# Kernel optimization log

Measured on AMD Instinct MI355X. Metric: run time of the kernel, lower is better.

Reference implementation:

```python
import jax, jax.numpy as jnp
import numpy as np

N_HEAD = 16

def setup_inputs() -> dict:
    key = jax.random.key(0)
    k1, k2, k3 = jax.random.split(key, 3)
    B, T, C = 4, 2048, 1024
    x = jax.random.normal(k1, (B, T, C), dtype=jnp.float32)
    W_attn = jax.random.normal(k2, (C, 3 * C), dtype=jnp.float32) * (1.0 / np.sqrt(C))
    W_proj = jax.random.normal(k3, (C, C), dtype=jnp.float32) * (1.0 / np.sqrt(C))
    return {"x": x, "W_attn": W_attn, "W_proj": W_proj}

def reference(x, W_attn, W_proj):
    B, T, C = x.shape
    H = N_HEAD
    D = C // H  # head_dim
    qkv = x @ W_attn                      # (B, T, 3C)
    q, k, v = jnp.split(qkv, 3, axis=-1)
    # (B, T, C) -> (B, H, T, D)
    q = q.reshape(B, T, H, D).transpose(0, 2, 1, 3)
    k = k.reshape(B, T, H, D).transpose(0, 2, 1, 3)
    v = v.reshape(B, T, H, D).transpose(0, 2, 1, 3)
    scale = 1.0 / np.sqrt(D)
    att = jnp.einsum('bhqd,bhkd->bhqk', q, k) * scale  # (B, H, T, T)
    causal = jnp.tril(jnp.ones((T, T), dtype=bool))
    att = jnp.where(causal[None, None, :, :], att, -jnp.inf)
    att = jax.nn.softmax(att, axis=-1)
    y = jnp.einsum('bhqk,bhkd->bhqd', att, v)          # (B, H, T, D)
    y = y.transpose(0, 2, 1, 3).reshape(B, T, C)
    y = y @ W_proj
    return y
```

## Files before the change

kernel.cpp:

```cpp
#include <hip/hip_runtime.h>
#include <hip/hip_bf16.h>
#include <stdint.h>

typedef __attribute__((ext_vector_type(8))) __bf16 bf16x8;
typedef __attribute__((ext_vector_type(4))) __bf16 bf16x4;
typedef __attribute__((ext_vector_type(4))) float f32x4;

static __device__ __forceinline__ ushort f2bf(float f) {
  union { float f; uint32_t u; } v; v.f = f;
  uint32_t u = v.u;
  u += 0x7fffu + ((u >> 16) & 1u);
  return (ushort)(u >> 16);
}

static __device__ __forceinline__ void gl_lds16(const ushort* g, ushort* l) {
  __builtin_amdgcn_global_load_lds(
      (__attribute__((address_space(1))) unsigned int*)(g),
      (__attribute__((address_space(3))) unsigned int*)(l), 16, 0, 0);
}

__global__ __launch_bounds__(256) void cast_f32_bf16(
    const float* __restrict__ in, ushort* __restrict__ out, int n) {
  int i = (blockIdx.x * 256 + threadIdx.x) * 4;
  if (i >= n) return;
  float4 v = *(const float4*)&in[i];
  ushort4 o;
  o.x = f2bf(v.x); o.y = f2bf(v.y); o.z = f2bf(v.z); o.w = f2bf(v.w);
  *(ushort4*)&out[i] = o;
}

__global__ __launch_bounds__(256) void transpose_cast(
    const float* __restrict__ W, ushort* __restrict__ Wt, int K, int N) {
  __shared__ ushort tile[32][33];
  int n0 = blockIdx.x * 32, k0 = blockIdx.y * 32;
  int tx = threadIdx.x, ty = threadIdx.y;
  #pragma unroll
  for (int r = ty; r < 32; r += 8)
    tile[r][tx] = f2bf(W[(size_t)(k0 + r) * N + n0 + tx]);
  __syncthreads();
  #pragma unroll
  for (int r = ty; r < 32; r += 8)
    Wt[(size_t)(n0 + r) * K + k0 + tx] = tile[tx][r];
}

template <int MODE>
__global__ __launch_bounds__(512, 2) void gemm_bt(
    const ushort* __restrict__ A, const ushort* __restrict__ Bt,
    float* __restrict__ Cf, int M, int N, int K,
    ushort* __restrict__ Qo, ushort* __restrict__ Ko, ushort* __restrict__ Vo) {
  __shared__ ushort smem[49152];
  const int tid = threadIdx.x;
  const int lane = tid & 63;
  const int w = tid >> 6;
  const int wm = (w >> 2) * 128;
  const int wn = (w & 3) * 32;
  const int lr = lane & 15, kg = lane >> 4;
  const int fid = blockIdx.x;
  const int m0 = (((fid & 7) << 2) + ((fid >> 3) & 3)) << 8;
  const int n0 = (fid >> 5) << 7;

  auto stageA = [&](int buf, int tile, int q) {
    const int k0 = tile << 6;
    const int rowb = q * 32 + (w >> 2) * 128 + (w & 3) * 8;
    gl_lds16(&A[(size_t)(m0 + rowb + (lane >> 3)) * K + k0 +
                (((lane & 7) ^ (lane >> 3)) << 3)],
             &smem[buf * 16384 + rowb * 64]);
  };
  auto stageB = [&](int buf, int tile, int h) {
    const int k0 = tile << 6;
    const int rowb = h * 64 + w * 8;
    gl_lds16(&Bt[(size_t)(n0 + rowb + (lane >> 3)) * K + k0 +
                 (((lane & 7) ^ (lane >> 3)) << 3)],
             &smem[32768 + buf * 8192 + rowb * 64]);
  };

  f32x4 zero = {0.f, 0.f, 0.f, 0.f};
  f32x4 acc[8][2];
  #pragma unroll
  for (int i = 0; i < 8; i++)
    #pragma unroll
    for (int j = 0; j < 2; j++) acc[i][j] = zero;

  const int cs0 = ((kg ^ (lr & 7)) << 3);
  const int cs1 = (((4 + kg) ^ (lr & 7)) << 3);

  const int nt = K >> 6;
  stageA(0, 0, 0); stageA(0, 0, 1); stageA(0, 0, 2); stageA(0, 0, 3);
  stageB(0, 0, 0); stageB(0, 0, 1);
  stageA(1, 1, 0); stageA(1, 1, 1); stageA(1, 1, 2);
  stageB(1, 1, 0); stageB(1, 1, 1);

  for (int t = 0; t < nt; ++t) {
    const int cur = t & 1, nxt = cur ^ 1;
    const int ab = cur * 16384, bb = 32768 + cur * 8192;
    if (t + 1 < nt)
      asm volatile("s_waitcnt vmcnt(5)" ::: "memory");
    else
      asm volatile("s_waitcnt vmcnt(0)" ::: "memory");
    __builtin_amdgcn_s_barrier();
    asm volatile("" ::: "memory");
    if (t + 1 < nt) stageA(nxt, t + 1, 3);
    bf16x8 bfr[2][2], af[2][2];
    #pragma unroll
    for (int j = 0; j < 2; ++j) {
      const int R = wn + j * 16 + lr;
      bfr[j][0] = *(const bf16x8*)&smem[bb + R * 64 + cs0];
      bfr[j][1] = *(const bf16x8*)&smem[bb + R * 64 + cs1];
    }
    #pragma unroll
    for (int il = 0; il < 2; ++il) {
      const int R = wm + il * 16 + lr;
      af[il][0] = *(const bf16x8*)&smem[ab + R * 64 + cs0];
      af[il][1] = *(const bf16x8*)&smem[ab + R * 64 + cs1];
    }
    asm volatile("s_waitcnt lgkmcnt(0)" ::: "memory");
    __builtin_amdgcn_sched_barrier(0);
    __builtin_amdgcn_s_setprio(1);
    #pragma unroll
    for (int il = 0; il < 2; ++il)
      #pragma unroll
      for (int j = 0; j < 2; ++j) {
        acc[il][j] = __builtin_amdgcn_mfma_f32_16x16x32_bf16(
            af[il][0], bfr[j][0], acc[il][j], 0, 0, 0);
        acc[il][j] = __builtin_amdgcn_mfma_f32_16x16x32_bf16(
            af[il][1], bfr[j][1], acc[il][j], 0, 0, 0);
      }
    __builtin_amdgcn_s_setprio(0);
    __builtin_amdgcn_s_barrier();
    asm volatile("" ::: "memory");
    #pragma unroll
    for (int p = 1; p < 4; ++p) {
      if (t + 2 < nt) {
        stageA(cur, t + 2, p - 1);
        if (p < 3) stageB(cur, t + 2, p - 1);
      }
      bf16x8 a2[2][2];
      #pragma unroll
      for (int il = 0; il < 2; ++il) {
        const int R = wm + (2 * p + il) * 16 + lr;
        a2[il][0] = *(const bf16x8*)&smem[ab + R * 64 + cs0];
        a2[il][1] = *(const bf16x8*)&smem[ab + R * 64 + cs1];
      }
      asm volatile("s_waitcnt lgkmcnt(0)" ::: "memory");
      __builtin_amdgcn_sched_barrier(0);
      __builtin_amdgcn_s_setprio(1);
      #pragma unroll
      for (int il = 0; il < 2; ++il)
        #pragma unroll
        for (int j = 0; j < 2; ++j) {
          acc[2 * p + il][j] = __builtin_amdgcn_mfma_f32_16x16x32_bf16(
              a2[il][0], bfr[j][0], acc[2 * p + il][j], 0, 0, 0);
          acc[2 * p + il][j] = __builtin_amdgcn_mfma_f32_16x16x32_bf16(
              a2[il][1], bfr[j][1], acc[2 * p + il][j], 0, 0, 0);
        }
      __builtin_amdgcn_s_setprio(0);
      __builtin_amdgcn_s_barrier();
      asm volatile("" ::: "memory");
    }
  }

  if (MODE == 2) {
    #pragma unroll
    for (int i = 0; i < 8; i++)
      #pragma unroll
      for (int j = 0; j < 2; j++)
        #pragma unroll
        for (int r = 0; r < 4; r++) {
          int mrow = m0 + wm + i * 16 + kg * 4 + r;
          int ncol = n0 + wn + j * 16 + lr;
          Cf[(size_t)mrow * N + ncol] = acc[i][j][r];
        }
  } else {
    __syncthreads();
    ushort* Ls = smem + w * 5120;
    const int nb = n0 + wn;
    const int which = nb >> 10;
    const int bb2 = (m0 + wm) >> 11;
    const int hh = (nb & 1023) >> 6;
    const int d0 = nb & 63;
    const size_t bh = (size_t)(bb2 * 16 + hh);
    const int t0 = (m0 + wm) & 2047;
    if (which == 2) {
      #pragma unroll
      for (int i = 0; i < 8; i++)
        #pragma unroll
        for (int j = 0; j < 2; j++)
          #pragma unroll
          for (int r = 0; r < 4; r++)
            Ls[(j * 16 + lr) * 136 + (i * 16 + kg * 4 + r)] =
                f2bf(acc[i][j][r]);
      #pragma unroll
      for (int it = 0; it < 8; it++) {
        const int cid = it * 64 + lane;
        const int d = cid >> 4, chk = cid & 15;
        bf16x8 v = *(const bf16x8*)&Ls[d * 136 + chk * 8];
        *(bf16x8*)&Vo[(bh * 64 + d0 + d) * 2048 + t0 + chk * 8] = v;
      }
    } else {
      const float sc = (which == 0) ? 0.18033688011112042f : 1.0f;
      #pragma unroll
      for (int i = 0; i < 8; i++)
        #pragma unroll
        for (int j = 0; j < 2; j++)
          #pragma unroll
          for (int r = 0; r < 4; r++)
            Ls[(i * 16 + kg * 4 + r) * 40 + (j * 16 + lr)] =
                f2bf(acc[i][j][r] * sc);
      ushort* dst = (which == 0) ? Qo : Ko;
      #pragma unroll
      for (int it = 0; it < 8; it++) {
        const int cid = it * 64 + lane;
        const int row = cid >> 2, chk = cid & 3;
        bf16x8 v = *(const bf16x8*)&Ls[row * 40 + chk * 8];
        *(bf16x8*)&dst[(bh * 2048 + t0 + row) * 64 + d0 + chk * 8] = v;
      }
    }
  }
}

__global__ __launch_bounds__(256, 4) void attn_fwd(
    const ushort* __restrict__ Q, const ushort* __restrict__ Kc,
    const ushort* __restrict__ Vt, ushort* __restrict__ Y) {
  __shared__ ushort Ks[2][64][64];
  __shared__ ushort Vs[2][64][64];
  __shared__ ushort Ps[4][16][64];
  const int tid = threadIdx.x;
  const int lane = tid & 63, w = tid >> 6;
  const int lr = lane & 15, kg = lane >> 4;
  int blk = blockIdx.x;
  blk = (blk & 7) * 128 + (blk >> 3);
  const int pair = blk & 15;
  const int bh = blk >> 4;
  const ushort* Qp = Q + (size_t)bh * 2048 * 64;
  const ushort* Kp = Kc + (size_t)bh * 2048 * 64;
  const ushort* Vp = Vt + (size_t)bh * 64 * 2048;
  const int b = bh >> 4, h = bh & 15;
  const int swz = (lr & 14) << 3;
  char* PsB = (char*)&Ps[w][0][0];
  const int srow = lane >> 3, schunk = lane & 7;
  const int cs0 = (kg ^ (lr & 7)) << 3;
  const int cs1 = ((kg ^ 4) ^ (lr & 7)) << 3;
  f32x4 zero = {0.f, 0.f, 0.f, 0.f};

  auto stageKV = [&](int buf, int k0) {
    #pragma unroll
    for (int c = 0; c < 2; c++) {
      const int rbase = w * 16 + c * 8;
      const int r = rbase + srow;
      gl_lds16(&Kp[(size_t)(k0 + r) * 64 + ((schunk ^ (r & 7)) << 3)],
               &Ks[buf][rbase][0]);
      gl_lds16(&Vp[(size_t)r * 2048 + k0 + ((schunk ^ (r & 7)) << 3)],
               &Vs[buf][rbase][0]);
    }
  };

  for (int half = 0; half < 2; half++) {
    const int j = half ? (31 - pair) : pair;
    const int q0b = j << 6;
    const int qw0 = q0b + w * 16;
    bf16x8 qf0 = *(const bf16x8*)&Qp[(size_t)(qw0 + lr) * 64 + kg * 8];
    bf16x8 qf1 = *(const bf16x8*)&Qp[(size_t)(qw0 + lr) * 64 + 32 + kg * 8];
    f32x4 o[4];
    #pragma unroll
    for (int dt = 0; dt < 4; dt++) o[dt] = zero;
    float lsum = 0.f;

    stageKV(0, 0);
    __syncthreads();
    for (int k0 = 0; k0 <= q0b; k0 += 64) {
      const int cur = (k0 >> 6) & 1;
      if (k0 < q0b) stageKV(cur ^ 1, k0 + 64);

      f32x4 s[4];
      #pragma unroll
      for (int ct = 0; ct < 4; ct++) {
        bf16x8 kf0 = *(const bf16x8*)&Ks[cur][ct * 16 + lr][cs0];
        bf16x8 kf1 = *(const bf16x8*)&Ks[cur][ct * 16 + lr][cs1];
        f32x4 z = zero;
        z = __builtin_amdgcn_mfma_f32_16x16x32_bf16(kf0, qf0, z, 0, 0, 0);
        z = __builtin_amdgcn_mfma_f32_16x16x32_bf16(kf1, qf1, z, 0, 0, 0);
        s[ct] = z;
      }
      if (k0 == q0b) {
        const int qrow = qw0 + lr;
        #pragma unroll
        for (int ct = 0; ct < 4; ct++)
          #pragma unroll
          for (int r = 0; r < 4; r++) {
            int kj = k0 + ct * 16 + kg * 4 + r;
            s[ct][r] = (kj > qrow) ? -1e30f : s[ct][r];
          }
      }
      #pragma unroll
      for (int ct = 0; ct < 4; ct++) {
        float p0 = exp2f(s[ct][0]);
        float p1 = exp2f(s[ct][1]);
        float p2 = exp2f(s[ct][2]);
        float p3 = exp2f(s[ct][3]);
        lsum += (p0 + p1) + (p2 + p3);
        bf16x4 pk = {(__bf16)p0, (__bf16)p1, (__bf16)p2, (__bf16)p3};
        *(bf16x4*)(PsB + lr * 128 + ((ct * 32 + kg * 8) ^ swz)) = pk;
      }
      bf16x8 pa0 = *(const bf16x8*)(PsB + lr * 128 + ((kg * 16) ^ swz));
      bf16x8 pa1 = *(const bf16x8*)(PsB + lr * 128 + ((64 + kg * 16) ^ swz));
      #pragma unroll
      for (int dt = 0; dt < 4; dt++) {
        bf16x8 vf0 = *(const bf16x8*)&Vs[cur][dt * 16 + lr][cs0];
        bf16x8 vf1 = *(const bf16x8*)&Vs[cur][dt * 16 + lr][cs1];
        f32x4 t = o[dt];
        t = __builtin_amdgcn_mfma_f32_16x16x32_bf16(pa0, vf0, t, 0, 0, 0);
        t = __builtin_amdgcn_mfma_f32_16x16x32_bf16(pa1, vf1, t, 0, 0, 0);
        o[dt] = t;
      }
      __syncthreads();
    }

    lsum += __shfl_xor(lsum, 16);
    lsum += __shfl_xor(lsum, 32);
    float inv = 1.f / lsum;
    f32x4 ib;
    #pragma unroll
    for (int r = 0; r < 4; r++) ib[r] = __shfl(inv, kg * 4 + r);
    #pragma unroll
    for (int dt = 0; dt < 4; dt++) {
      #pragma unroll
      for (int r = 0; r < 4; r++) {
        size_t t = (size_t)qw0 + kg * 4 + r;
        Y[((size_t)b * 2048 + t) * 1024 + h * 64 + dt * 16 + lr] =
            f2bf(o[dt][r] * ib[r]);
      }
    }
  }
}

extern "C" void kernel_launch(void* const* d_in, const int* in_sizes, int n_in,
                              void* d_out, int out_size, void* d_ws,
                              size_t ws_size, hipStream_t stream) {
  const float* x = (const float*)d_in[0];
  const float* Wa = (const float*)d_in[1];
  const float* Wp = (const float*)d_in[2];
  float* out = (float*)d_out;

  char* ws = (char*)d_ws;
  size_t off = 0;
  auto carve = [&](size_t bytes) {
    void* p = ws + off;
    off += (bytes + 255) & ~(size_t)255;
    return p;
  };
  ushort* Xb = (ushort*)carve(8192ull * 1024 * 2);
  ushort* Wat = (ushort*)carve(3072ull * 1024 * 2);
  ushort* Wpt = (ushort*)carve(1024ull * 1024 * 2);
  ushort* Qh = (ushort*)carve(64ull * 2048 * 64 * 2);
  ushort* Kh = (ushort*)carve(64ull * 2048 * 64 * 2);
  ushort* Vt = (ushort*)carve(64ull * 64 * 2048 * 2);
  ushort* Yb = (ushort*)carve(8192ull * 1024 * 2);

  cast_f32_bf16<<<8192, 256, 0, stream>>>(x, Xb, 8192 * 1024);
  transpose_cast<<<dim3(96, 32), dim3(32, 8), 0, stream>>>(Wa, Wat, 1024, 3072);
  transpose_cast<<<dim3(32, 32), dim3(32, 8), 0, stream>>>(Wp, Wpt, 1024, 1024);
  gemm_bt<1><<<768, 512, 0, stream>>>(Xb, Wat, nullptr, 8192, 3072, 1024, Qh,
                                      Kh, Vt);
  attn_fwd<<<1024, 256, 0, stream>>>(Qh, Kh, Vt, Yb);
  gemm_bt<2><<<256, 512, 0, stream>>>(Yb, Wpt, out, 8192, 1024, 1024, nullptr,
                                      nullptr, nullptr);
}
```

Before: 177.0 us.

## Shrink GEMM tiles to 128x128 with 4 waves and restructure pipeline

Changes the GEMM from 256x128 tiles with 8 waves to 128x128 tiles with 4 waves, each wave computing a 64x64 sub-tile. The grid doubles, and the software pipeline is reorganised into two half-phases that alternate loading A and B. The epilogue now writes full 64-wide head chunks to Q/K/V. The goal is more blocks for better CU load balance and a larger per-wave tile for register reuse, at the cost of lower arithmetic intensity per block and more global traffic.

```diff
diff --git a/kernel.cpp b/kernel.cpp
--- a/kernel.cpp
+++ b/kernel.cpp
@@ -44,68 +44,69 @@
 }
 
 template <int MODE>
-__global__ __launch_bounds__(512, 2) void gemm_bt(
+__global__ __launch_bounds__(256, 2) void gemm_bt(
     const ushort* __restrict__ A, const ushort* __restrict__ Bt,
     float* __restrict__ Cf, int M, int N, int K,
     ushort* __restrict__ Qo, ushort* __restrict__ Ko, ushort* __restrict__ Vo) {
-  __shared__ ushort smem[49152];
+  __shared__ ushort smem[32768];
   const int tid = threadIdx.x;
   const int lane = tid & 63;
   const int w = tid >> 6;
-  const int wm = (w >> 2) * 128;
-  const int wn = (w & 3) * 32;
+  const int wm = (w >> 1) * 64, wn = (w & 1) * 64;
   const int lr = lane & 15, kg = lane >> 4;
   const int fid = blockIdx.x;
-  const int m0 = (((fid & 7) << 2) + ((fid >> 3) & 3)) << 8;
-  const int n0 = (fid >> 5) << 7;
+  const int m0 = (((fid & 7) << 3) + ((fid >> 3) & 7)) << 7;
+  const int n0 = (fid >> 6) << 7;
 
   auto stageA = [&](int buf, int tile, int q) {
     const int k0 = tile << 6;
-    const int rowb = q * 32 + (w >> 2) * 128 + (w & 3) * 8;
+    const int rowb = q * 32 + w * 8;
     gl_lds16(&A[(size_t)(m0 + rowb + (lane >> 3)) * K + k0 +
                 (((lane & 7) ^ (lane >> 3)) << 3)],
-             &smem[buf * 16384 + rowb * 64]);
+             &smem[buf * 8192 + rowb * 64]);
   };
-  auto stageB = [&](int buf, int tile, int h) {
+  auto stageB = [&](int buf, int tile, int q) {
     const int k0 = tile << 6;
-    const int rowb = h * 64 + w * 8;
+    const int rowb = q * 32 + w * 8;
     gl_lds16(&Bt[(size_t)(n0 + rowb + (lane >> 3)) * K + k0 +
                  (((lane & 7) ^ (lane >> 3)) << 3)],
-             &smem[32768 + buf * 8192 + rowb * 64]);
+             &smem[16384 + buf * 8192 + rowb * 64]);
   };
 
   f32x4 zero = {0.f, 0.f, 0.f, 0.f};
-  f32x4 acc[8][2];
+  f32x4 acc[4][4];
   #pragma unroll
-  for (int i = 0; i < 8; i++)
-    #pragma unroll
-    for (int j = 0; j < 2; j++) acc[i][j] = zero;
+  for (int i = 0; i < 4; i++)
+    #pragma unroll
+    for (int j = 0; j < 4; j++) acc[i][j] = zero;
 
   const int cs0 = ((kg ^ (lr & 7)) << 3);
   const int cs1 = (((4 + kg) ^ (lr & 7)) << 3);
 
   const int nt = K >> 6;
+  stageB(0, 0, 0); stageB(0, 0, 1); stageB(0, 0, 2); stageB(0, 0, 3);
   stageA(0, 0, 0); stageA(0, 0, 1); stageA(0, 0, 2); stageA(0, 0, 3);
-  stageB(0, 0, 0); stageB(0, 0, 1);
-  stageA(1, 1, 0); stageA(1, 1, 1); stageA(1, 1, 2);
-  stageB(1, 1, 0); stageB(1, 1, 1);
+  stageB(1, 1, 0); stageB(1, 1, 1); stageB(1, 1, 2); stageB(1, 1, 3);
 
   for (int t = 0; t < nt; ++t) {
     const int cur = t & 1, nxt = cur ^ 1;
-    const int ab = cur * 16384, bb = 32768 + cur * 8192;
+    const int ab = cur * 8192, bbo = 16384 + cur * 8192;
     if (t + 1 < nt)
-      asm volatile("s_waitcnt vmcnt(5)" ::: "memory");
+      asm volatile("s_waitcnt vmcnt(4)" ::: "memory");
     else
       asm volatile("s_waitcnt vmcnt(0)" ::: "memory");
     __builtin_amdgcn_s_barrier();
     asm volatile("" ::: "memory");
-    if (t + 1 < nt) stageA(nxt, t + 1, 3);
-    bf16x8 bfr[2][2], af[2][2];
-    #pragma unroll
-    for (int j = 0; j < 2; ++j) {
+    if (t + 1 < nt) {
+      stageA(nxt, t + 1, 0); stageA(nxt, t + 1, 1);
+      stageA(nxt, t + 1, 2); stageA(nxt, t + 1, 3);
+    }
+    bf16x8 bfr[4][2], af[2][2];
+    #pragma unroll
+    for (int j = 0; j < 4; ++j) {
       const int R = wn + j * 16 + lr;
-      bfr[j][0] = *(const bf16x8*)&smem[bb + R * 64 + cs0];
-      bfr[j][1] = *(const bf16x8*)&smem[bb + R * 64 + cs1];
+      bfr[j][0] = *(const bf16x8*)&smem[bbo + R * 64 + cs0];
+      bfr[j][1] = *(const bf16x8*)&smem[bbo + R * 64 + cs1];
     }
     #pragma unroll
     for (int il = 0; il < 2; ++il) {
@@ -119,7 +120,7 @@
     #pragma unroll
     for (int il = 0; il < 2; ++il)
       #pragma unroll
-      for (int j = 0; j < 2; ++j) {
+      for (int j = 0; j < 4; ++j) {
         acc[il][j] = __builtin_amdgcn_mfma_f32_16x16x32_bf16(
             af[il][0], bfr[j][0], acc[il][j], 0, 0, 0);
         acc[il][j] = __builtin_amdgcn_mfma_f32_16x16x32_bf16(
@@ -128,42 +129,37 @@
     __builtin_amdgcn_s_setprio(0);
     __builtin_amdgcn_s_barrier();
     asm volatile("" ::: "memory");
-    #pragma unroll
-    for (int p = 1; p < 4; ++p) {
-      if (t + 2 < nt) {
-        stageA(cur, t + 2, p - 1);
-        if (p < 3) stageB(cur, t + 2, p - 1);
-      }
-      bf16x8 a2[2][2];
-      #pragma unroll
-      for (int il = 0; il < 2; ++il) {
-        const int R = wm + (2 * p + il) * 16 + lr;
-        a2[il][0] = *(const bf16x8*)&smem[ab + R * 64 + cs0];
-        a2[il][1] = *(const bf16x8*)&smem[ab + R * 64 + cs1];
-      }
-      asm volatile("s_waitcnt lgkmcnt(0)" ::: "memory");
-      __builtin_amdgcn_sched_barrier(0);
-      __builtin_amdgcn_s_setprio(1);
-      #pragma unroll
-      for (int il = 0; il < 2; ++il)
-        #pragma unroll
-        for (int j = 0; j < 2; ++j) {
-          acc[2 * p + il][j] = __builtin_amdgcn_mfma_f32_16x16x32_bf16(
-              a2[il][0], bfr[j][0], acc[2 * p + il][j], 0, 0, 0);
-          acc[2 * p + il][j] = __builtin_amdgcn_mfma_f32_16x16x32_bf16(
-              a2[il][1], bfr[j][1], acc[2 * p + il][j], 0, 0, 0);
-        }
-      __builtin_amdgcn_s_setprio(0);
-      __builtin_amdgcn_s_barrier();
-      asm volatile("" ::: "memory");
-    }
+    if (t + 2 < nt) {
+      stageB(cur, t + 2, 0); stageB(cur, t + 2, 1);
+      stageB(cur, t + 2, 2); stageB(cur, t + 2, 3);
+    }
+    bf16x8 a2[2][2];
+    #pragma unroll
+    for (int il = 0; il < 2; ++il) {
+      const int R = wm + (2 + il) * 16 + lr;
+      a2[il][0] = *(const bf16x8*)&smem[ab + R * 64 + cs0];
+      a2[il][1] = *(const bf16x8*)&smem[ab + R * 64 + cs1];
+    }
+    asm volatile("s_waitcnt lgkmcnt(0)" ::: "memory");
+    __builtin_amdgcn_sched_barrier(0);
+    __builtin_amdgcn_s_setprio(1);
+    #pragma unroll
+    for (int il = 0; il < 2; ++il)
+      #pragma unroll
+      for (int j = 0; j < 4; ++j) {
+        acc[2 + il][j] = __builtin_amdgcn_mfma_f32_16x16x32_bf16(
+            a2[il][0], bfr[j][0], acc[2 + il][j], 0, 0, 0);
+        acc[2 + il][j] = __builtin_amdgcn_mfma_f32_16x16x32_bf16(
+            a2[il][1], bfr[j][1], acc[2 + il][j], 0, 0, 0);
+      }
+    __builtin_amdgcn_s_setprio(0);
   }
 
   if (MODE == 2) {
     #pragma unroll
-    for (int i = 0; i < 8; i++)
-      #pragma unroll
-      for (int j = 0; j < 2; j++)
+    for (int i = 0; i < 4; i++)
+      #pragma unroll
+      for (int j = 0; j < 4; j++)
         #pragma unroll
         for (int r = 0; r < 4; r++) {
           int mrow = m0 + wm + i * 16 + kg * 4 + r;
@@ -172,47 +168,46 @@
         }
   } else {
     __syncthreads();
-    ushort* Ls = smem + w * 5120;
+    ushort* Ls = smem + w * 4608;
     const int nb = n0 + wn;
     const int which = nb >> 10;
     const int bb2 = (m0 + wm) >> 11;
     const int hh = (nb & 1023) >> 6;
-    const int d0 = nb & 63;
     const size_t bh = (size_t)(bb2 * 16 + hh);
     const int t0 = (m0 + wm) & 2047;
     if (which == 2) {
       #pragma unroll
-      for (int i = 0; i < 8; i++)
+      for (int i = 0; i < 4; i++)
         #pragma unroll
-        for (int j = 0; j < 2; j++)
+        for (int j = 0; j < 4; j++)
           #pragma unroll
           for (int r = 0; r < 4; r++)
-            Ls[(j * 16 + lr) * 136 + (i * 16 + kg * 4 + r)] =
+            Ls[(j * 16 + lr) * 72 + (i * 16 + kg * 4 + r)] =
                 f2bf(acc[i][j][r]);
       #pragma unroll
       for (int it = 0; it < 8; it++) {
         const int cid = it * 64 + lane;
-        const int d = cid >> 4, chk = cid & 15;
-        bf16x8 v = *(const bf16x8*)&Ls[d * 136 + chk * 8];
-        *(bf16x8*)&Vo[(bh * 64 + d0 + d) * 2048 + t0 + chk * 8] = v;
+        const int d = cid >> 3, chk = cid & 7;
+        bf16x8 v = *(const bf16x8*)&Ls[d * 72 + chk * 8];
+        *(bf16x8*)&Vo[(bh * 64 + d) * 2048 + t0 + chk * 8] = v;
       }
     } else {
       const float sc = (which == 0) ? 0.18033688011112042f : 1.0f;
       #pragma unroll
-      for (int i = 0; i < 8; i++)
+      for (int i = 0; i < 4; i++)
         #pragma unroll
-        for (int j = 0; j < 2; j++)
+        for (int j = 0; j < 4; j++)
           #pragma unroll
           for (int r = 0; r < 4; r++)
-            Ls[(i * 16 + kg * 4 + r) * 40 + (j * 16 + lr)] =
+            Ls[(i * 16 + kg * 4 + r) * 72 + (j * 16 + lr)] =
                 f2bf(acc[i][j][r] * sc);
       ushort* dst = (which == 0) ? Qo : Ko;
       #pragma unroll
       for (int it = 0; it < 8; it++) {
         const int cid = it * 64 + lane;
-        const int row = cid >> 2, chk = cid & 3;
-        bf16x8 v = *(const bf16x8*)&Ls[row * 40 + chk * 8];
-        *(bf16x8*)&dst[(bh * 2048 + t0 + row) * 64 + d0 + chk * 8] = v;
+        const int row = cid >> 3, chk = cid & 7;
+        bf16x8 v = *(const bf16x8*)&Ls[row * 72 + chk * 8];
+        *(bf16x8*)&dst[(bh * 2048 + t0 + row) * 64 + chk * 8] = v;
       }
     }
   }
@@ -359,9 +354,9 @@
   cast_f32_bf16<<<8192, 256, 0, stream>>>(x, Xb, 8192 * 1024);
   transpose_cast<<<dim3(96, 32), dim3(32, 8), 0, stream>>>(Wa, Wat, 1024, 3072);
   transpose_cast<<<dim3(32, 32), dim3(32, 8), 0, stream>>>(Wp, Wpt, 1024, 1024);
-  gemm_bt<1><<<768, 512, 0, stream>>>(Xb, Wat, nullptr, 8192, 3072, 1024, Qh,
-                                      Kh, Vt);
+  gemm_bt<1><<<1536, 256, 0, stream>>>(Xb, Wat, nullptr, 8192, 3072, 1024, Qh,
+                                       Kh, Vt);
   attn_fwd<<<1024, 256, 0, stream>>>(Qh, Kh, Vt, Yb);
-  gemm_bt<2><<<256, 512, 0, stream>>>(Yb, Wpt, out, 8192, 1024, 1024, nullptr,
+  gemm_bt<2><<<512, 256, 0, stream>>>(Yb, Wpt, out, 8192, 1024, 1024, nullptr,
                                       nullptr, nullptr);
 }
```

After: 169.1 us. 4.5% less time.
